# Kernel optimization log

Measured on AMD Instinct MI355X. Metric: run time of the kernel, lower is better.

The kernel has to match this reference:

```python
import jax, jax.numpy as jnp
import numpy as np

ENC, PRED, H, V, DMAX = 1024, 640, 640, 1024, 4
B, T, U = 4, 256, 64


def setup_inputs() -> dict:
    key = jax.random.key(0)
    ks = jax.random.split(key, 10)
    s = lambda d: 1.0 / np.sqrt(d)
    return {
        "encoder_out": jax.random.normal(ks[0], (B, T, ENC), jnp.float32),
        "predictor_out": jax.random.normal(ks[1], (B, U, PRED), jnp.float32),
        "W_enc": jax.random.uniform(ks[2], (H, ENC), jnp.float32, -s(ENC), s(ENC)),
        "b_enc": jax.random.uniform(ks[3], (H,), jnp.float32, -s(ENC), s(ENC)),
        "W_pred": jax.random.uniform(ks[4], (H, PRED), jnp.float32, -s(PRED), s(PRED)),
        "b_pred": jax.random.uniform(ks[5], (H,), jnp.float32, -s(PRED), s(PRED)),
        "W_out": jax.random.uniform(ks[6], (V, H), jnp.float32, -s(H), s(H)),
        "b_out": jax.random.uniform(ks[7], (V,), jnp.float32, -s(H), s(H)),
        "W_dur": jax.random.uniform(ks[8], (DMAX + 1, H), jnp.float32, -s(H), s(H)),
        "b_dur": jax.random.uniform(ks[9], (DMAX + 1,), jnp.float32, -s(H), s(H)),
    }


def reference(encoder_out, predictor_out, W_enc, b_enc, W_pred, b_pred,
              W_out, b_out, W_dur, b_dur):
    # Project encoder [B,T,H] and predictor [B,U,H]
    enc = jnp.einsum('bte,he->bth', encoder_out, W_enc) + b_enc
    pred = jnp.einsum('bup,hp->buh', predictor_out, W_pred) + b_pred
    # Broadcast-add -> [B,T,U,H], tanh
    joint = jnp.tanh(enc[:, :, None, :] + pred[:, None, :, :])
    # Dual heads
    logits = jnp.einsum('btuh,vh->btuv', joint, W_out) + b_out        # [B,T,U,V]
    durations = jnp.einsum('btuh,dh->btud', joint, W_dur) + b_dur     # [B,T,U,DMAX+1]
    return (logits, durations)
```

## Files before the change

kernel.cpp:

```cpp
#include <hip/hip_runtime.h>

typedef unsigned short u16;
typedef unsigned int u32;

typedef __bf16 bf16x8 __attribute__((ext_vector_type(8)));
typedef float f32x4 __attribute__((ext_vector_type(4)));

union FragI { int4 i; bf16x8 b; u16 u[8]; };

__device__ __forceinline__ u16 f2bf(float x) {
  u32 u = __float_as_uint(x);
  u32 r = (u + 0x7fffu + ((u >> 16) & 1u)) >> 16;
  return (u16)r;
}
__device__ __forceinline__ float tanh_fast(float x) {
  float e = __expf(2.0f * x);
  return 1.0f - __fdividef(2.0f, e + 1.0f);
}
__device__ __forceinline__ bf16x8 load_cvt8(const float* __restrict__ p) {
  float4 f0 = *(const float4*)p;
  float4 f1 = *(const float4*)(p + 4);
  union { bf16x8 b; u16 u[8]; } t;
  t.u[0] = f2bf(f0.x); t.u[1] = f2bf(f0.y); t.u[2] = f2bf(f0.z); t.u[3] = f2bf(f0.w);
  t.u[4] = f2bf(f1.x); t.u[5] = f2bf(f1.y); t.u[6] = f2bf(f1.z); t.u[7] = f2bf(f1.w);
  return t.b;
}

#define GLDS(gptr, lptr) \
  __builtin_amdgcn_global_load_lds((const __attribute__((address_space(1))) u32*)(gptr), \
                                   (__attribute__((address_space(3))) u32*)(lptr), 16, 0, 0)

__global__ __launch_bounds__(256) void conv_v4(const float* __restrict__ in,
                                               u16* __restrict__ out, int n4) {
  int i = blockIdx.x * 256 + threadIdx.x;
  if (i >= n4) return;
  float4 f = ((const float4*)in)[i];
  union { u16 u[4]; int2 v; } o;
  o.u[0] = f2bf(f.x); o.u[1] = f2bf(f.y); o.u[2] = f2bf(f.z); o.u[3] = f2bf(f.w);
  ((int2*)out)[i] = o.v;
}

__global__ __launch_bounds__(256) void conv_wdur(const float* __restrict__ in,
                                                 u16* __restrict__ out) {
  int i = blockIdx.x * 256 + threadIdx.x;
  if (i < 16 * 640) out[i] = (i < 5 * 640) ? f2bf(in[i]) : (u16)0;
}

__global__ __launch_bounds__(256) void proj_gemm(const float* __restrict__ A,
                                                 const float* __restrict__ Bw,
                                                 const float* __restrict__ bias,
                                                 float* __restrict__ C,
                                                 int M, int N, int K) {
  int tid = threadIdx.x;
  int lane = tid & 63, wid = tid >> 6;
  int m0 = blockIdx.x * 64, n0 = blockIdx.y * 64;
  int kper = K >> 2;
  int kbase = wid * kper;
  int ksteps = kper >> 5;
  int r16 = lane & 15, khi = (lane >> 4) * 8;

  f32x4 z = {0.f, 0.f, 0.f, 0.f};
  f32x4 acc[4][4];
  for (int i = 0; i < 4; ++i)
    for (int j = 0; j < 4; ++j) acc[i][j] = z;

  for (int ks = 0; ks < ksteps; ++ks) {
    int k = kbase + ks * 32 + khi;
    bf16x8 af[4], bf[4];
#pragma unroll
    for (int fm = 0; fm < 4; ++fm)
      af[fm] = load_cvt8(A + (size_t)(m0 + fm * 16 + r16) * K + k);
#pragma unroll
    for (int fn = 0; fn < 4; ++fn)
      bf[fn] = load_cvt8(Bw + (size_t)(n0 + fn * 16 + r16) * K + k);
#pragma unroll
    for (int fm = 0; fm < 4; ++fm)
#pragma unroll
      for (int fn = 0; fn < 4; ++fn)
        acc[fm][fn] = __builtin_amdgcn_mfma_f32_16x16x32_bf16(af[fm], bf[fn], acc[fm][fn], 0, 0, 0);
  }

  __shared__ float red[4][64][64];
#pragma unroll
  for (int fm = 0; fm < 4; ++fm)
#pragma unroll
    for (int fn = 0; fn < 4; ++fn)
#pragma unroll
      for (int i = 0; i < 4; ++i)
        red[wid][fm * 16 + (lane >> 4) * 4 + i][fn * 16 + r16] = acc[fm][fn][i];
  __syncthreads();
  for (int idx = tid; idx < 4096; idx += 256) {
    int r = idx >> 6, c = idx & 63;
    float s = red[0][r][c] + red[1][r][c] + red[2][r][c] + red[3][r][c] + bias[n0 + c];
    C[(size_t)(m0 + r) * N + n0 + c] = s;
  }
}

__global__ __launch_bounds__(256) void joint_tanh(const float* __restrict__ enc,
                                                  const float* __restrict__ pred,
                                                  u16* __restrict__ J) {
  const int total = 65536 * 80;
  for (int c = blockIdx.x * 256 + threadIdx.x; c < total; c += gridDim.x * 256) {
    int m = c / 80;
    int j = c - m * 80;
    int bt = m >> 6;
    int uu = m & 63;
    int b = bt >> 8;
    const float* ep = enc + bt * 640 + j * 8;
    const float* pp = pred + (b * 64 + uu) * 640 + j * 8;
    float4 e0 = *(const float4*)ep;
    float4 e1 = *(const float4*)(ep + 4);
    float4 p0 = *(const float4*)pp;
    float4 p1 = *(const float4*)(pp + 4);
    union { u16 u[8]; int4 v; } o;
    o.u[0] = f2bf(tanh_fast(e0.x + p0.x));
    o.u[1] = f2bf(tanh_fast(e0.y + p0.y));
    o.u[2] = f2bf(tanh_fast(e0.z + p0.z));
    o.u[3] = f2bf(tanh_fast(e0.w + p0.w));
    o.u[4] = f2bf(tanh_fast(e1.x + p1.x));
    o.u[5] = f2bf(tanh_fast(e1.y + p1.y));
    o.u[6] = f2bf(tanh_fast(e1.z + p1.z));
    o.u[7] = f2bf(tanh_fast(e1.w + p1.w));
    *(int4*)(J + (size_t)c * 8) = o.v;
  }
}

#define LOGITS_N 67108864

__device__ __forceinline__ void stage128(const u16* __restrict__ g, u16* l,
                                         int wid, int lane) {
  int rl = wid * 8 + (lane >> 3);
  int cl = ((lane & 7) ^ (lane >> 3)) * 8;
  const u16* gp = g + (size_t)rl * 640 + cl;
  u16* lp = l + wid * 512;
#pragma unroll
  for (int j = 0; j < 4; ++j)
    GLDS(gp + (size_t)j * 32 * 640, lp + j * 2048);
}

__global__ __launch_bounds__(256, 3) void main_gemm(const u16* __restrict__ J,
                                                    const u16* __restrict__ Wo,
                                                    const u16* __restrict__ Wd,
                                                    const float* __restrict__ b_out,
                                                    const float* __restrict__ b_dur,
                                                    float* __restrict__ out) {
  __shared__ __align__(16) u16 As[8192];
  __shared__ __align__(16) u16 Bs[8192];
  int tid = threadIdx.x;
  int lane = tid & 63, wid = tid >> 6;
  int bid = blockIdx.x;
  int swz = (bid & 7) * 512 + (bid >> 3);
  int bn = swz & 7, bm = swz >> 3;
  int m0 = bm * 128, n0 = bn * 128;
  int wr = wid >> 1, wc = wid & 1;
  int r16 = lane & 15, khi = (lane >> 4) * 8;
  int xorv = (r16 & 7) << 3;
  bool do_dur = (bn == 0);

  f32x4 z = {0.f, 0.f, 0.f, 0.f};
  f32x4 acc[4][4];
#pragma unroll
  for (int i = 0; i < 4; ++i)
#pragma unroll
    for (int j = 0; j < 4; ++j) acc[i][j] = z;
  f32x4 dacc[4] = {z, z, z, z};

  const u16* Jb = J + (size_t)m0 * 640;
  const u16* Wb = Wo + (size_t)n0 * 640;

  for (int t = 0; t < 10; ++t) {
    stage128(Jb + t * 64, As, wid, lane);
    stage128(Wb + t * 64, Bs, wid, lane);
    __syncthreads();
#pragma unroll
    for (int ks = 0; ks < 2; ++ks) {
      int cks = (ks * 32 + khi) ^ xorv;
      FragI af[4], bfr[4], wd;
#pragma unroll
      for (int fn = 0; fn < 4; ++fn)
        bfr[fn].i = *(const int4*)(Bs + (wc * 64 + fn * 16 + r16) * 64 + cks);
#pragma unroll
      for (int fm = 0; fm < 4; ++fm)
        af[fm].i = *(const int4*)(As + (wr * 64 + fm * 16 + r16) * 64 + cks);
      if (do_dur)
        wd.i = *(const int4*)(Wd + (size_t)r16 * 640 + t * 64 + ks * 32 + khi);
#pragma unroll
      for (int fm = 0; fm < 4; ++fm) {
#pragma unroll
        for (int fn = 0; fn < 4; ++fn)
          acc[fm][fn] = __builtin_amdgcn_mfma_f32_16x16x32_bf16(af[fm].b, bfr[fn].b, acc[fm][fn], 0, 0, 0);
        if (do_dur)
          dacc[fm] = __builtin_amdgcn_mfma_f32_16x16x32_bf16(af[fm].b, wd.b, dacc[fm], 0, 0, 0);
      }
    }
    __syncthreads();
  }

  int rb = m0 + wr * 64 + (lane >> 4) * 4;
  int cb = n0 + wc * 64 + r16;
#pragma unroll
  for (int fn = 0; fn < 4; ++fn) {
    int col = cb + fn * 16;
    float bo = b_out[col];
#pragma unroll
    for (int fm = 0; fm < 4; ++fm) {
      int row = rb + fm * 16;
#pragma unroll
      for (int i = 0; i < 4; ++i)
        out[(size_t)(row + i) * 1024 + col] = acc[fm][fn][i] + bo;
    }
  }
  if (do_dur && r16 < 5) {
    float bd = b_dur[r16];
#pragma unroll
    for (int fm = 0; fm < 4; ++fm) {
      int row = rb + fm * 16;
#pragma unroll
      for (int i = 0; i < 4; ++i)
        out[LOGITS_N + (size_t)(row + i) * 5 + r16] = dacc[fm][i] + bd;
    }
  }
}

extern "C" void kernel_launch(void* const* d_in, const int* in_sizes, int n_in,
                              void* d_out, int out_size, void* d_ws, size_t ws_size,
                              hipStream_t stream) {
  const float* encoder   = (const float*)d_in[0];
  const float* predictor = (const float*)d_in[1];
  const float* W_enc = (const float*)d_in[2];
  const float* b_enc = (const float*)d_in[3];
  const float* W_pred = (const float*)d_in[4];
  const float* b_pred = (const float*)d_in[5];
  const float* W_out = (const float*)d_in[6];
  const float* b_out = (const float*)d_in[7];
  const float* W_dur = (const float*)d_in[8];
  const float* b_dur = (const float*)d_in[9];
  float* out = (float*)d_out;

  char* ws = (char*)d_ws;
  u16* Jbuf    = (u16*)(ws);
  u16* WoutB   = (u16*)(ws + 83886080);
  u16* WdurB   = (u16*)(ws + 85196800);
  float* encP  = (float*)(ws + 85217280);
  float* predP = (float*)(ws + 87838720);

  conv_v4<<<640, 256, 0, stream>>>(W_out, WoutB, 163840);
  conv_wdur<<<40, 256, 0, stream>>>(W_dur, WdurB);
  proj_gemm<<<dim3(16, 10), 256, 0, stream>>>(encoder, W_enc, b_enc, encP, 1024, 640, 1024);
  proj_gemm<<<dim3(4, 10), 256, 0, stream>>>(predictor, W_pred, b_pred, predP, 256, 640, 640);
  joint_tanh<<<2048, 256, 0, stream>>>(encP, predP, Jbuf);
  main_gemm<<<4096, 256, 0, stream>>>(Jbuf, WoutB, WdurB, b_out, b_dur, out);
}
```

Baseline: 179.1 us.

## Move duration head into joint tanh kernel and drop it from main GEMM

The duration head is now computed in the joint kernel: each wave builds one joint row, writes the bf16 copy, and does 5 fp32 dot products with W_dur using wave shuffle reductions. The main GEMM loses the bn==0 branch with its extra MFMAs and global W_dur loads, which removes the load imbalance across blocks and lets launch bounds rise to 4 blocks per SM. The cost is more work in the joint kernel: shuffle reductions and W_dur reads for every row, plus narrower 2-float loads and stores.

```diff
diff --git a/kernel.cpp b/kernel.cpp
--- a/kernel.cpp
+++ b/kernel.cpp
@@ -29,6 +29,8 @@
 #define GLDS(gptr, lptr) \
   __builtin_amdgcn_global_load_lds((const __attribute__((address_space(1))) u32*)(gptr), \
                                    (__attribute__((address_space(3))) u32*)(lptr), 16, 0, 0)
+
+#define LOGITS_N 67108864
 
 __global__ __launch_bounds__(256) void conv_v4(const float* __restrict__ in,
                                                u16* __restrict__ out, int n4) {
@@ -38,12 +40,6 @@
   union { u16 u[4]; int2 v; } o;
   o.u[0] = f2bf(f.x); o.u[1] = f2bf(f.y); o.u[2] = f2bf(f.z); o.u[3] = f2bf(f.w);
   ((int2*)out)[i] = o.v;
-}
-
-__global__ __launch_bounds__(256) void conv_wdur(const float* __restrict__ in,
-                                                 u16* __restrict__ out) {
-  int i = blockIdx.x * 256 + threadIdx.x;
-  if (i < 16 * 640) out[i] = (i < 5 * 640) ? f2bf(in[i]) : (u16)0;
 }
 
 __global__ __launch_bounds__(256) void proj_gemm(const float* __restrict__ A,
@@ -96,36 +92,47 @@
   }
 }
 
-__global__ __launch_bounds__(256) void joint_tanh(const float* __restrict__ enc,
-                                                  const float* __restrict__ pred,
-                                                  u16* __restrict__ J) {
-  const int total = 65536 * 80;
-  for (int c = blockIdx.x * 256 + threadIdx.x; c < total; c += gridDim.x * 256) {
-    int m = c / 80;
-    int j = c - m * 80;
-    int bt = m >> 6;
-    int uu = m & 63;
-    int b = bt >> 8;
-    const float* ep = enc + bt * 640 + j * 8;
-    const float* pp = pred + (b * 64 + uu) * 640 + j * 8;
-    float4 e0 = *(const float4*)ep;
-    float4 e1 = *(const float4*)(ep + 4);
-    float4 p0 = *(const float4*)pp;
-    float4 p1 = *(const float4*)(pp + 4);
-    union { u16 u[8]; int4 v; } o;
-    o.u[0] = f2bf(tanh_fast(e0.x + p0.x));
-    o.u[1] = f2bf(tanh_fast(e0.y + p0.y));
-    o.u[2] = f2bf(tanh_fast(e0.z + p0.z));
-    o.u[3] = f2bf(tanh_fast(e0.w + p0.w));
-    o.u[4] = f2bf(tanh_fast(e1.x + p1.x));
-    o.u[5] = f2bf(tanh_fast(e1.y + p1.y));
-    o.u[6] = f2bf(tanh_fast(e1.z + p1.z));
-    o.u[7] = f2bf(tanh_fast(e1.w + p1.w));
-    *(int4*)(J + (size_t)c * 8) = o.v;
-  }
-}
-
-#define LOGITS_N 67108864
+__global__ __launch_bounds__(256) void joint_dur(const float* __restrict__ enc,
+                                                 const float* __restrict__ pred,
+                                                 const float* __restrict__ W_dur,
+                                                 const float* __restrict__ b_dur,
+                                                 u16* __restrict__ J,
+                                                 float* __restrict__ out) {
+  int lane = threadIdx.x & 63, w = threadIdx.x >> 6;
+  int m = blockIdx.x * 4 + w;
+  int bt = m >> 6, uu = m & 63;
+  int b = bt >> 8;
+  const float* ep = enc + (size_t)bt * 640 + lane * 2;
+  const float* pp = pred + (size_t)(b * 64 + uu) * 640 + lane * 2;
+  u16* jp = J + (size_t)m * 640 + lane * 2;
+
+  float v0[5], v1[5];
+#pragma unroll
+  for (int i = 0; i < 5; ++i) {
+    float2 e = *(const float2*)(ep + i * 128);
+    float2 p = *(const float2*)(pp + i * 128);
+    v0[i] = tanh_fast(e.x + p.x);
+    v1[i] = tanh_fast(e.y + p.y);
+    u32 pk = (u32)f2bf(v0[i]) | ((u32)f2bf(v1[i]) << 16);
+    *(u32*)(jp + i * 128) = pk;
+  }
+#pragma unroll
+  for (int j = 0; j < 5; ++j) {
+    const float* wp = W_dur + j * 640 + lane * 2;
+    float s = 0.f;
+#pragma unroll
+    for (int i = 0; i < 5; ++i) {
+      float2 wv = *(const float2*)(wp + i * 128);
+      s += v0[i] * wv.x + v1[i] * wv.y;
+    }
+#pragma unroll
+    for (int off = 1; off < 64; off <<= 1)
+      s += __shfl_xor(s, off, 64);
+    if (lane == j)
+      out[LOGITS_N + (size_t)m * 5 + j] = s + b_dur[j];
+  }
+}
+
 
 __device__ __forceinline__ void stage128(const u16* __restrict__ g, u16* l,
                                          int wid, int lane) {
@@ -138,11 +145,9 @@
     GLDS(gp + (size_t)j * 32 * 640, lp + j * 2048);
 }
 
-__global__ __launch_bounds__(256, 3) void main_gemm(const u16* __restrict__ J,
+__global__ __launch_bounds__(256, 4) void main_gemm(const u16* __restrict__ J,
                                                     const u16* __restrict__ Wo,
-                                                    const u16* __restrict__ Wd,
                                                     const float* __restrict__ b_out,
-                                                    const float* __restrict__ b_dur,
                                                     float* __restrict__ out) {
   __shared__ __align__(16) u16 As[8192];
   __shared__ __align__(16) u16 Bs[8192];
@@ -155,7 +160,6 @@
   int wr = wid >> 1, wc = wid & 1;
   int r16 = lane & 15, khi = (lane >> 4) * 8;
   int xorv = (r16 & 7) << 3;
-  bool do_dur = (bn == 0);
 
   f32x4 z = {0.f, 0.f, 0.f, 0.f};
   f32x4 acc[4][4];
@@ -163,7 +167,6 @@
   for (int i = 0; i < 4; ++i)
 #pragma unroll
     for (int j = 0; j < 4; ++j) acc[i][j] = z;
-  f32x4 dacc[4] = {z, z, z, z};
 
   const u16* Jb = J + (size_t)m0 * 640;
   const u16* Wb = Wo + (size_t)n0 * 640;
@@ -175,23 +178,18 @@
 #pragma unroll
     for (int ks = 0; ks < 2; ++ks) {
       int cks = (ks * 32 + khi) ^ xorv;
-      FragI af[4], bfr[4], wd;
+      FragI af[4], bfr[4];
 #pragma unroll
       for (int fn = 0; fn < 4; ++fn)
         bfr[fn].i = *(const int4*)(Bs + (wc * 64 + fn * 16 + r16) * 64 + cks);
 #pragma unroll
       for (int fm = 0; fm < 4; ++fm)
         af[fm].i = *(const int4*)(As + (wr * 64 + fm * 16 + r16) * 64 + cks);
-      if (do_dur)
-        wd.i = *(const int4*)(Wd + (size_t)r16 * 640 + t * 64 + ks * 32 + khi);
-#pragma unroll
-      for (int fm = 0; fm < 4; ++fm) {
+#pragma unroll
+      for (int fm = 0; fm < 4; ++fm)
 #pragma unroll
         for (int fn = 0; fn < 4; ++fn)
           acc[fm][fn] = __builtin_amdgcn_mfma_f32_16x16x32_bf16(af[fm].b, bfr[fn].b, acc[fm][fn], 0, 0, 0);
-        if (do_dur)
-          dacc[fm] = __builtin_amdgcn_mfma_f32_16x16x32_bf16(af[fm].b, wd.b, dacc[fm], 0, 0, 0);
-      }
     }
     __syncthreads();
   }
@@ -208,16 +206,6 @@
 #pragma unroll
       for (int i = 0; i < 4; ++i)
         out[(size_t)(row + i) * 1024 + col] = acc[fm][fn][i] + bo;
-    }
-  }
-  if (do_dur && r16 < 5) {
-    float bd = b_dur[r16];
-#pragma unroll
-    for (int fm = 0; fm < 4; ++fm) {
-      int row = rb + fm * 16;
-#pragma unroll
-      for (int i = 0; i < 4; ++i)
-        out[LOGITS_N + (size_t)(row + i) * 5 + r16] = dacc[fm][i] + bd;
     }
   }
 }
@@ -240,14 +228,12 @@
   char* ws = (char*)d_ws;
   u16* Jbuf    = (u16*)(ws);
   u16* WoutB   = (u16*)(ws + 83886080);
-  u16* WdurB   = (u16*)(ws + 85196800);
-  float* encP  = (float*)(ws + 85217280);
-  float* predP = (float*)(ws + 87838720);
+  float* encP  = (float*)(ws + 85196800);
+  float* predP = (float*)(ws + 87818240);
 
   conv_v4<<<640, 256, 0, stream>>>(W_out, WoutB, 163840);
-  conv_wdur<<<40, 256, 0, stream>>>(W_dur, WdurB);
   proj_gemm<<<dim3(16, 10), 256, 0, stream>>>(encoder, W_enc, b_enc, encP, 1024, 640, 1024);
   proj_gemm<<<dim3(4, 10), 256, 0, stream>>>(predictor, W_pred, b_pred, predP, 256, 640, 640);
-  joint_tanh<<<2048, 256, 0, stream>>>(encP, predP, Jbuf);
-  main_gemm<<<4096, 256, 0, stream>>>(Jbuf, WoutB, WdurB, b_out, b_dur, out);
-}
+  joint_dur<<<16384, 256, 0, stream>>>(encP, predP, W_dur, b_dur, Jbuf, out);
+  main_gemm<<<4096, 256, 0, stream>>>(Jbuf, WoutB, b_out, out);
+}
```

Result: slower. 216.2 us (+20.7%).

## Split duration head into separate kernel and raise main GEMM occupancy

Applied to the files above, without the earlier changes.

Moves the duration-head MFMA computation out of the main logits GEMM into a dedicated small kernel that streams the joint tensor directly from global memory. This removes the duration accumulators and branch from the main kernel, allowing launch bounds to request 4 blocks per CU instead of 3 and balancing work across blocks. The cost is an extra full read of the bf16 joint tensor and an additional kernel launch.

```diff
diff --git a/kernel.cpp b/kernel.cpp
--- a/kernel.cpp
+++ b/kernel.cpp
@@ -29,6 +29,8 @@
 #define GLDS(gptr, lptr) \
   __builtin_amdgcn_global_load_lds((const __attribute__((address_space(1))) u32*)(gptr), \
                                    (__attribute__((address_space(3))) u32*)(lptr), 16, 0, 0)
+
+#define LOGITS_N 67108864
 
 __global__ __launch_bounds__(256) void conv_v4(const float* __restrict__ in,
                                                u16* __restrict__ out, int n4) {
@@ -125,7 +127,32 @@
   }
 }
 
-#define LOGITS_N 67108864
+__global__ __launch_bounds__(256) void dur_gemm(const u16* __restrict__ J,
+                                                const u16* __restrict__ WdB,
+                                                const float* __restrict__ b_dur,
+                                                float* __restrict__ out) {
+  int lane = threadIdx.x & 63, wid = threadIdx.x >> 6;
+  int r16 = lane & 15, g4 = lane >> 4;
+  int khi8 = g4 * 8;
+  int row0 = blockIdx.x * 64 + wid * 16;
+  const u16* Ap = J + (size_t)(row0 + r16) * 640 + khi8;
+  const u16* Wp = WdB + (size_t)r16 * 640 + khi8;
+  f32x4 dacc = {0.f, 0.f, 0.f, 0.f};
+#pragma unroll 4
+  for (int kof = 0; kof < 640; kof += 32) {
+    FragI af, wd;
+    af.i = *(const int4*)(Ap + kof);
+    wd.i = *(const int4*)(Wp + kof);
+    dacc = __builtin_amdgcn_mfma_f32_16x16x32_bf16(af.b, wd.b, dacc, 0, 0, 0);
+  }
+  if (r16 < 5) {
+    float bd = b_dur[r16];
+#pragma unroll
+    for (int i = 0; i < 4; ++i)
+      out[LOGITS_N + (size_t)(row0 + g4 * 4 + i) * 5 + r16] = dacc[i] + bd;
+  }
+}
+
 
 __device__ __forceinline__ void stage128(const u16* __restrict__ g, u16* l,
                                          int wid, int lane) {
@@ -138,11 +165,9 @@
     GLDS(gp + (size_t)j * 32 * 640, lp + j * 2048);
 }
 
-__global__ __launch_bounds__(256, 3) void main_gemm(const u16* __restrict__ J,
+__global__ __launch_bounds__(256, 4) void main_gemm(const u16* __restrict__ J,
                                                     const u16* __restrict__ Wo,
-                                                    const u16* __restrict__ Wd,
                                                     const float* __restrict__ b_out,
-                                                    const float* __restrict__ b_dur,
                                                     float* __restrict__ out) {
   __shared__ __align__(16) u16 As[8192];
   __shared__ __align__(16) u16 Bs[8192];
@@ -155,7 +180,6 @@
   int wr = wid >> 1, wc = wid & 1;
   int r16 = lane & 15, khi = (lane >> 4) * 8;
   int xorv = (r16 & 7) << 3;
-  bool do_dur = (bn == 0);
 
   f32x4 z = {0.f, 0.f, 0.f, 0.f};
   f32x4 acc[4][4];
@@ -163,7 +187,6 @@
   for (int i = 0; i < 4; ++i)
 #pragma unroll
     for (int j = 0; j < 4; ++j) acc[i][j] = z;
-  f32x4 dacc[4] = {z, z, z, z};
 
   const u16* Jb = J + (size_t)m0 * 640;
   const u16* Wb = Wo + (size_t)n0 * 640;
@@ -175,23 +198,18 @@
 #pragma unroll
     for (int ks = 0; ks < 2; ++ks) {
       int cks = (ks * 32 + khi) ^ xorv;
-      FragI af[4], bfr[4], wd;
+      FragI af[4], bfr[4];
 #pragma unroll
       for (int fn = 0; fn < 4; ++fn)
         bfr[fn].i = *(const int4*)(Bs + (wc * 64 + fn * 16 + r16) * 64 + cks);
 #pragma unroll
       for (int fm = 0; fm < 4; ++fm)
         af[fm].i = *(const int4*)(As + (wr * 64 + fm * 16 + r16) * 64 + cks);
-      if (do_dur)
-        wd.i = *(const int4*)(Wd + (size_t)r16 * 640 + t * 64 + ks * 32 + khi);
-#pragma unroll
-      for (int fm = 0; fm < 4; ++fm) {
+#pragma unroll
+      for (int fm = 0; fm < 4; ++fm)
 #pragma unroll
         for (int fn = 0; fn < 4; ++fn)
           acc[fm][fn] = __builtin_amdgcn_mfma_f32_16x16x32_bf16(af[fm].b, bfr[fn].b, acc[fm][fn], 0, 0, 0);
-        if (do_dur)
-          dacc[fm] = __builtin_amdgcn_mfma_f32_16x16x32_bf16(af[fm].b, wd.b, dacc[fm], 0, 0, 0);
-      }
     }
     __syncthreads();
   }
@@ -208,16 +226,6 @@
 #pragma unroll
       for (int i = 0; i < 4; ++i)
         out[(size_t)(row + i) * 1024 + col] = acc[fm][fn][i] + bo;
-    }
-  }
-  if (do_dur && r16 < 5) {
-    float bd = b_dur[r16];
-#pragma unroll
-    for (int fm = 0; fm < 4; ++fm) {
-      int row = rb + fm * 16;
-#pragma unroll
-      for (int i = 0; i < 4; ++i)
-        out[LOGITS_N + (size_t)(row + i) * 5 + r16] = dacc[fm][i] + bd;
     }
   }
 }
@@ -249,5 +257,6 @@
   proj_gemm<<<dim3(16, 10), 256, 0, stream>>>(encoder, W_enc, b_enc, encP, 1024, 640, 1024);
   proj_gemm<<<dim3(4, 10), 256, 0, stream>>>(predictor, W_pred, b_pred, predP, 256, 640, 640);
   joint_tanh<<<2048, 256, 0, stream>>>(encP, predP, Jbuf);
-  main_gemm<<<4096, 256, 0, stream>>>(Jbuf, WoutB, WdurB, b_out, b_dur, out);
-}
+  dur_gemm<<<1024, 256, 0, stream>>>(Jbuf, WdurB, b_dur, out);
+  main_gemm<<<4096, 256, 0, stream>>>(Jbuf, WoutB, b_out, out);
+}
```

Measured after the change: 194.0 us. 8.3% more time.
